# Performance work log

Measured on AMD Instinct MI355X. Metric: run time of the kernel, lower is better.

The kernel has to match this reference:

```python
import jax, jax.numpy as jnp
import numpy as np
from math import sqrt


def setup_inputs() -> dict:
    key0 = jax.random.key(0)
    ks = jax.random.split(key0, 7)
    N, H, E, D, S = 32, 16, 128, 128, 2047
    return {
        "query": jax.random.normal(ks[0], (N, H, E), dtype=jnp.float32),
        "key": jax.random.normal(ks[1], (N, H, E), dtype=jnp.float32),
        "value": jax.random.normal(ks[2], (N, H, D), dtype=jnp.float32),
        "keys_cache": jax.random.normal(ks[3], (N, H, S, E), dtype=jnp.float32),
        "values_cache": jax.random.normal(ks[4], (N, H, S, D), dtype=jnp.float32),
        "w_pre": jax.random.normal(ks[5], (H, H), dtype=jnp.float32) * (1.0 / sqrt(H)),
        "w_post": jax.random.normal(ks[6], (H, H), dtype=jnp.float32) * (1.0 / sqrt(H)),
    }


def reference(query, key, value, keys_cache, values_cache, w_pre, w_post):
    # Single recurrent decode step with talking-heads mixing (dropout in eval mode).
    N, H, E = query.shape
    softmax_temp = 1.0 / sqrt(E)
    # Append current key/value to the cache: [N,H,S+1,E] / [N,H,S+1,D]
    keys = jnp.concatenate([keys_cache, key[:, :, None, :]], axis=2)
    values = jnp.concatenate([values_cache, value[:, :, None, :]], axis=2)
    # Scores: [N,H,S]
    QK = jnp.einsum('nhe,nhse->nhs', query, keys)
    # Pre-softmax talking heads (1x1 conv over head axis): out_g = sum_h w[g,h] * in_h
    QK = jnp.einsum('gh,nhs->ngs', w_pre, QK)
    A = jax.nn.softmax(softmax_temp * QK, axis=-1)
    # Post-softmax talking heads
    A = jnp.einsum('gh,nhs->ngs', w_post, A)
    # Weighted value readout: [N,H,D]
    V = jnp.einsum('nhs,nhsd->nhd', A, values)
    return V, keys, values
```

## Files before the change

kernel.cpp:

```cpp
#include <hip/hip_runtime.h>
#include <cstddef>

constexpr int N_  = 32;
constexpr int H_  = 16;
constexpr int E_  = 128;
constexpr int D_  = 128;
constexpr int S_  = 2047;
constexpr int SP1 = 2048;
constexpr int NH  = N_ * H_;

constexpr int ROWS_PER_BLOCK = 256;
constexpr int CHUNKS = SP1 / ROWS_PER_BLOCK;
constexpr int COLCH  = SP1 / 256;

typedef float vfloat4 __attribute__((ext_vector_type(4)));

__global__ __launch_bounds__(256) void k1_keys_scores(
    const float* __restrict__ query, const float* __restrict__ key,
    const float* __restrict__ keys_cache,
    float* __restrict__ keys_out, float* __restrict__ scores)
{
  __shared__ float sc[ROWS_PER_BLOCK];
  const int bid   = blockIdx.x;
  const int nh    = bid / CHUNKS;
  const int chunk = bid % CHUNKS;
  const int tid   = threadIdx.x;
  const int wave  = tid >> 6;
  const int lane  = tid & 63;
  const int half  = lane >> 5;
  const int lcol  = lane & 31;
  const int rbase = wave * 64 + half;

  const vfloat4 q4 = *reinterpret_cast<const vfloat4*>(query + (size_t)nh * E_ + lcol * 4);

  #pragma unroll
  for (int it8 = 0; it8 < 4; ++it8) {
    vfloat4 v[8];
    #pragma unroll
    for (int j = 0; j < 8; ++j) {
      const int r = rbase + (it8 * 8 + j) * 2;
      const int s = chunk * ROWS_PER_BLOCK + r;
      const float* src = (s < S_) ? (keys_cache + ((size_t)nh * S_ + s) * E_)
                                  : (key + (size_t)nh * E_);
      v[j] = __builtin_nontemporal_load(
          reinterpret_cast<const vfloat4*>(src + lcol * 4));
    }
    #pragma unroll
    for (int j = 0; j < 8; ++j) {
      const int r = rbase + (it8 * 8 + j) * 2;
      const int s = chunk * ROWS_PER_BLOCK + r;
      __builtin_nontemporal_store(v[j],
          reinterpret_cast<vfloat4*>(keys_out + ((size_t)nh * SP1 + s) * E_ + lcol * 4));

      float p = q4.x * v[j].x + q4.y * v[j].y + q4.z * v[j].z + q4.w * v[j].w;
      p += __shfl_xor(p, 1);
      p += __shfl_xor(p, 2);
      p += __shfl_xor(p, 4);
      p += __shfl_xor(p, 8);
      p += __shfl_xor(p, 16);
      if (lcol == 0) sc[r] = p;
    }
  }
  __syncthreads();
  scores[(size_t)nh * SP1 + chunk * ROWS_PER_BLOCK + tid] = sc[tid];
}

__global__ __launch_bounds__(256) void k2a_stats(
    const float* __restrict__ scores, const float* __restrict__ w_pre,
    float* __restrict__ blkstats)
{
  __shared__ float wp[H_ * H_];
  __shared__ float red[4][H_];
  __shared__ float bmax[H_];
  const int n   = blockIdx.x >> 3;
  const int cc  = blockIdx.x & 7;
  const int tid = threadIdx.x;
  const int wave = tid >> 6;
  const int lane = tid & 63;
  const float temp = 0.08838834764831845f;

  wp[tid] = w_pre[tid];
  __syncthreads();

  const float* base = scores + (size_t)n * H_ * SP1 + cc * 256 + tid;
  float sc[H_];
  #pragma unroll
  for (int h = 0; h < H_; ++h) sc[h] = base[(size_t)h * SP1];

  float mx[H_];
  #pragma unroll
  for (int g = 0; g < H_; ++g) {
    float acc = 0.0f;
    #pragma unroll
    for (int h = 0; h < H_; ++h) acc += wp[g * H_ + h] * sc[h];
    mx[g] = acc * temp;
  }

  #pragma unroll
  for (int g = 0; g < H_; ++g) {
    float v = mx[g];
    #pragma unroll
    for (int m = 1; m <= 32; m <<= 1) v = fmaxf(v, __shfl_xor(v, m));
    if (lane == 0) red[wave][g] = v;
  }
  __syncthreads();
  if (tid < H_) {
    float v = fmaxf(fmaxf(red[0][tid], red[1][tid]), fmaxf(red[2][tid], red[3][tid]));
    bmax[tid] = v;
    blkstats[((size_t)(n * COLCH + cc) * 2 + 0) * H_ + tid] = v;
  }
  __syncthreads();

  #pragma unroll
  for (int g = 0; g < H_; ++g) {
    float e = __expf(mx[g] - bmax[g]);
    #pragma unroll
    for (int m = 1; m <= 32; m <<= 1) e += __shfl_xor(e, m);
    if (lane == 0) red[wave][g] = e;
  }
  __syncthreads();
  if (tid < H_) {
    blkstats[((size_t)(n * COLCH + cc) * 2 + 1) * H_ + tid] =
        red[0][tid] + red[1][tid] + red[2][tid] + red[3][tid];
  }
}

__global__ __launch_bounds__(256) void k2c_a2(
    const float* __restrict__ scores, const float* __restrict__ blkstats,
    const float* __restrict__ w_pre, const float* __restrict__ w_post,
    float* __restrict__ a2out)
{
  __shared__ float wp[H_ * H_];
  __shared__ float wq[H_ * H_];
  __shared__ float mg[H_];
  __shared__ float ig[H_];
  const int n   = blockIdx.x >> 3;
  const int cc  = blockIdx.x & 7;
  const int tid = threadIdx.x;
  const float temp = 0.08838834764831845f;

  wp[tid] = w_pre[tid];
  wq[tid] = w_post[tid];
  if (tid < H_) {
    float bm[COLCH], bs[COLCH];
    #pragma unroll
    for (int c = 0; c < COLCH; ++c) {
      bm[c] = blkstats[((size_t)(n * COLCH + c) * 2 + 0) * H_ + tid];
      bs[c] = blkstats[((size_t)(n * COLCH + c) * 2 + 1) * H_ + tid];
    }
    float m = bm[0];
    #pragma unroll
    for (int c = 1; c < COLCH; ++c) m = fmaxf(m, bm[c]);
    float den = 0.0f;
    #pragma unroll
    for (int c = 0; c < COLCH; ++c) den += bs[c] * __expf(bm[c] - m);
    mg[tid] = m;
    ig[tid] = 1.0f / den;
  }
  __syncthreads();

  const float* base = scores + (size_t)n * H_ * SP1 + cc * 256 + tid;
  float sc[H_];
  #pragma unroll
  for (int h = 0; h < H_; ++h) sc[h] = base[(size_t)h * SP1];

  float P[H_];
  #pragma unroll
  for (int h = 0; h < H_; ++h) {
    float acc = 0.0f;
    #pragma unroll
    for (int h2 = 0; h2 < H_; ++h2) acc += wp[h * H_ + h2] * sc[h2];
    P[h] = __expf(acc * temp - mg[h]) * ig[h];
  }

  #pragma unroll
  for (int g = 0; g < H_; ++g) {
    float a = 0.0f;
    #pragma unroll
    for (int h = 0; h < H_; ++h) a += wq[g * H_ + h] * P[h];
    a2out[((size_t)(n * H_ + g)) * SP1 + cc * 256 + tid] = a;
  }
}

__global__ __launch_bounds__(256) void k3_values(
    const float* __restrict__ value, const float* __restrict__ values_cache,
    const float* __restrict__ a2buf, float* __restrict__ values_out,
    float* __restrict__ partials)
{
  __shared__ float lds[8][128];
  __shared__ float a2[ROWS_PER_BLOCK];
  const int bid   = blockIdx.x;
  const int nh    = bid / CHUNKS;
  const int chunk = bid % CHUNKS;
  const int tid   = threadIdx.x;
  const int wave  = tid >> 6;
  const int lane  = tid & 63;
  const int half  = lane >> 5;
  const int lcol  = lane & 31;
  const int group = wave * 2 + half;
  const int rbase = wave * 64 + half;

  a2[tid] = a2buf[(size_t)nh * SP1 + chunk * ROWS_PER_BLOCK + tid];
  __syncthreads();

  float accx = 0.0f, accy = 0.0f, accz = 0.0f, accw = 0.0f;

  #pragma unroll
  for (int it8 = 0; it8 < 4; ++it8) {
    vfloat4 v[8];
    #pragma unroll
    for (int j = 0; j < 8; ++j) {
      const int r = rbase + (it8 * 8 + j) * 2;
      const int s = chunk * ROWS_PER_BLOCK + r;
      const float* src = (s < S_) ? (values_cache + ((size_t)nh * S_ + s) * D_)
                                  : (value + (size_t)nh * D_);
      v[j] = __builtin_nontemporal_load(
          reinterpret_cast<const vfloat4*>(src + lcol * 4));
    }
    #pragma unroll
    for (int j = 0; j < 8; ++j) {
      const int r = rbase + (it8 * 8 + j) * 2;
      const int s = chunk * ROWS_PER_BLOCK + r;
      __builtin_nontemporal_store(v[j],
          reinterpret_cast<vfloat4*>(values_out + ((size_t)nh * SP1 + s) * D_ + lcol * 4));

      const float w = a2[r];
      accx += w * v[j].x;
      accy += w * v[j].y;
      accz += w * v[j].z;
      accw += w * v[j].w;
    }
  }

  lds[group][lcol * 4 + 0] = accx;
  lds[group][lcol * 4 + 1] = accy;
  lds[group][lcol * 4 + 2] = accz;
  lds[group][lcol * 4 + 3] = accw;
  __syncthreads();
  if (tid < 128) {
    float sum = 0.0f;
    #pragma unroll
    for (int gq = 0; gq < 8; ++gq) sum += lds[gq][tid];
    partials[(size_t)bid * 128 + tid] = sum;
  }
}

__global__ __launch_bounds__(256) void k4_reduce(
    const float* __restrict__ partials, float* __restrict__ v_out)
{
  const int g = blockIdx.x * 256 + threadIdx.x;
  const int nh = g >> 7;
  const int d = g & 127;
  float s = 0.0f;
  #pragma unroll
  for (int c = 0; c < CHUNKS; ++c)
    s += partials[((size_t)(nh * CHUNKS + c)) * 128 + d];
  v_out[g] = s;
}

extern "C" void kernel_launch(void* const* d_in, const int* in_sizes, int n_in,
                              void* d_out, int out_size, void* d_ws, size_t ws_size,
                              hipStream_t stream) {
  const float* query        = (const float*)d_in[0];
  const float* key          = (const float*)d_in[1];
  const float* value        = (const float*)d_in[2];
  const float* keys_cache   = (const float*)d_in[3];
  const float* values_cache = (const float*)d_in[4];
  const float* w_pre        = (const float*)d_in[5];
  const float* w_post       = (const float*)d_in[6];

  float* out = (float*)d_out;
  float* v_out      = out;
  float* keys_out   = out + (size_t)NH * D_;
  float* values_out = keys_out + (size_t)NH * SP1 * E_;

  float* buf0     = (float*)d_ws;
  float* a2buf    = buf0 + (size_t)NH * SP1;
  float* blkstats = a2buf + (size_t)NH * SP1;
  float* partials = blkstats + (size_t)N_ * COLCH * 2 * H_;

  k1_keys_scores<<<NH * CHUNKS, 256, 0, stream>>>(query, key, keys_cache,
                                                  keys_out, buf0);
  k2a_stats<<<N_ * COLCH, 256, 0, stream>>>(buf0, w_pre, blkstats);
  k2c_a2<<<N_ * COLCH, 256, 0, stream>>>(buf0, blkstats, w_pre, w_post, a2buf);
  k3_values<<<NH * CHUNKS, 256, 0, stream>>>(value, values_cache, a2buf,
                                             values_out, partials);
  k4_reduce<<<(NH * 128) / 256, 256, 0, stream>>>(partials, v_out);
}
```

Before: 384.8 us.

## Process full sequence per block in k3 and drop separate reduce kernel

The values kernel now assigns one block per (n,h) pair and loops over all 2048 rows, instead of splitting each pair into 8 chunks. It writes the final readout directly, which removes the partials buffer and the k4_reduce launch. This cuts one kernel launch and the partial-sum traffic. In exchange the grid shrinks from 4096 to 512 blocks, and each block streams 1 MB, which may leave too little memory parallelism on a 256-CU device for this bandwidth-bound copy.

```diff
diff --git a/kernel.cpp b/kernel.cpp
--- a/kernel.cpp
+++ b/kernel.cpp
@@ -185,33 +185,32 @@
 __global__ __launch_bounds__(256) void k3_values(
     const float* __restrict__ value, const float* __restrict__ values_cache,
     const float* __restrict__ a2buf, float* __restrict__ values_out,
-    float* __restrict__ partials)
+    float* __restrict__ v_out)
 {
   __shared__ float lds[8][128];
-  __shared__ float a2[ROWS_PER_BLOCK];
-  const int bid   = blockIdx.x;
-  const int nh    = bid / CHUNKS;
-  const int chunk = bid % CHUNKS;
+  __shared__ float a2[SP1];
+  const int nh    = blockIdx.x;
   const int tid   = threadIdx.x;
   const int wave  = tid >> 6;
   const int lane  = tid & 63;
   const int half  = lane >> 5;
   const int lcol  = lane & 31;
   const int group = wave * 2 + half;
-  const int rbase = wave * 64 + half;
-
-  a2[tid] = a2buf[(size_t)nh * SP1 + chunk * ROWS_PER_BLOCK + tid];
+
+  #pragma unroll
+  for (int k = 0; k < SP1 / 256; ++k)
+    a2[tid + k * 256] = a2buf[(size_t)nh * SP1 + tid + k * 256];
   __syncthreads();
 
   float accx = 0.0f, accy = 0.0f, accz = 0.0f, accw = 0.0f;
 
-  #pragma unroll
-  for (int it8 = 0; it8 < 4; ++it8) {
+  const int rbase = wave * 512 + half;
+  #pragma unroll 4
+  for (int it8 = 0; it8 < 32; ++it8) {
     vfloat4 v[8];
     #pragma unroll
     for (int j = 0; j < 8; ++j) {
-      const int r = rbase + (it8 * 8 + j) * 2;
-      const int s = chunk * ROWS_PER_BLOCK + r;
+      const int s = rbase + (it8 * 8 + j) * 2;
       const float* src = (s < S_) ? (values_cache + ((size_t)nh * S_ + s) * D_)
                                   : (value + (size_t)nh * D_);
       v[j] = __builtin_nontemporal_load(
@@ -219,12 +218,11 @@
     }
     #pragma unroll
     for (int j = 0; j < 8; ++j) {
-      const int r = rbase + (it8 * 8 + j) * 2;
-      const int s = chunk * ROWS_PER_BLOCK + r;
+      const int s = rbase + (it8 * 8 + j) * 2;
       __builtin_nontemporal_store(v[j],
           reinterpret_cast<vfloat4*>(values_out + ((size_t)nh * SP1 + s) * D_ + lcol * 4));
 
-      const float w = a2[r];
+      const float w = a2[s];
       accx += w * v[j].x;
       accy += w * v[j].y;
       accz += w * v[j].z;
@@ -241,21 +239,8 @@
     float sum = 0.0f;
     #pragma unroll
     for (int gq = 0; gq < 8; ++gq) sum += lds[gq][tid];
-    partials[(size_t)bid * 128 + tid] = sum;
-  }
-}
-
-__global__ __launch_bounds__(256) void k4_reduce(
-    const float* __restrict__ partials, float* __restrict__ v_out)
-{
-  const int g = blockIdx.x * 256 + threadIdx.x;
-  const int nh = g >> 7;
-  const int d = g & 127;
-  float s = 0.0f;
-  #pragma unroll
-  for (int c = 0; c < CHUNKS; ++c)
-    s += partials[((size_t)(nh * CHUNKS + c)) * 128 + d];
-  v_out[g] = s;
+    v_out[(size_t)nh * 128 + tid] = sum;
+  }
 }
 
 extern "C" void kernel_launch(void* const* d_in, const int* in_sizes, int n_in,
@@ -277,13 +262,11 @@
   float* buf0     = (float*)d_ws;
   float* a2buf    = buf0 + (size_t)NH * SP1;
   float* blkstats = a2buf + (size_t)NH * SP1;
-  float* partials = blkstats + (size_t)N_ * COLCH * 2 * H_;
 
   k1_keys_scores<<<NH * CHUNKS, 256, 0, stream>>>(query, key, keys_cache,
                                                   keys_out, buf0);
   k2a_stats<<<N_ * COLCH, 256, 0, stream>>>(buf0, w_pre, blkstats);
   k2c_a2<<<N_ * COLCH, 256, 0, stream>>>(buf0, blkstats, w_pre, w_post, a2buf);
-  k3_values<<<NH * CHUNKS, 256, 0, stream>>>(value, values_cache, a2buf,
-                                             values_out, partials);
-  k4_reduce<<<(NH * 128) / 256, 256, 0, stream>>>(partials, v_out);
-}
+  k3_values<<<NH, 256, 0, stream>>>(value, values_cache, a2buf,
+                                    values_out, v_out);
+}
```

Measured after the change: 432.0 us. 12.3% more time.
